# Kernel tuning notes

Hardware: AMD Instinct MI355X
Metric: run time of the kernel (lower is better)

## Reference

```python
import jax, jax.numpy as jnp
import numpy as np
import math

D_MODEL = 768
NUM_HEADS = 8
D_ATT = D_MODEL // NUM_HEADS


def _pos_encoding(S):
    # pe: [S, d_model] sinusoidal, scaled by d_model**-0.5, reshaped to [h, S, d_att]
    position = jnp.arange(S, dtype=jnp.float32)[:, None]                      # [S,1]
    div_term = jnp.exp(jnp.arange(0, D_MODEL, 2, dtype=jnp.float32)
                       * (-math.log(10000.0) / D_MODEL))                      # [d_model/2]
    pe = jnp.zeros((S, D_MODEL), dtype=jnp.float32)
    pe = pe.at[:, 0::2].set(jnp.sin(position * div_term))
    pe = pe.at[:, 1::2].set(jnp.cos(position * div_term))
    pe = pe * (D_MODEL ** -0.5)
    return pe.reshape(S, NUM_HEADS, D_ATT).transpose(1, 0, 2)                 # [h,S,d]


def setup_inputs() -> dict:
    key = jax.random.key(0)
    k1, k2 = jax.random.split(key)
    B, S = 16, 4096
    src = jax.random.normal(k1, (B, S, D_MODEL), dtype=jnp.float32)
    src_key_padding_mask = jnp.zeros((B, S), dtype=bool)  # all valid
    query = jax.random.normal(k2, (NUM_HEADS, D_ATT), dtype=jnp.float32) * (D_ATT ** -0.5)
    return {"src": src, "src_key_padding_mask": src_key_padding_mask, "query": query}


def reference(src, src_key_padding_mask, query):
    B, S, C = src.shape
    key = src.reshape(B, S, NUM_HEADS, D_ATT).transpose(0, 2, 1, 3)          # [B,h,S,d]
    val = key + _pos_encoding(S)[None]                                        # [B,h,S,d]
    scores = jnp.einsum('hd,bhsd->bhs', query, key)                           # [B,h,S]
    scores = jnp.where(src_key_padding_mask[:, None, :], -jnp.inf, scores)
    weights = jax.nn.softmax(scores, axis=-1)                                 # [B,h,S]
    pooled = jnp.einsum('bhsd,bhs->bhd', val, weights)                        # [B,h,d]
    return pooled.reshape(B, NUM_HEADS * D_ATT)                               # [B,C]
```

## Files before the change

kernel.cpp:

```cpp
#include <hip/hip_runtime.h>
#include <math.h>

namespace {
constexpr int kB = 16;
constexpr int kS = 4096;
constexpr int kH = 8;
constexpr int kD = 96;
constexpr int kDM = 768;
constexpr int kNC = 64;
constexpr int kCS = kS / kNC;
constexpr int kRW = kCS / 4;
constexpr int kNSC2 = 32;
constexpr int kS2 = kS / kNSC2;
constexpr float kPeScale = 0.03608439182435161f;
constexpr float kNegLog = -9.210340371976184f / 768.0f;
constexpr float kHalfPi = 1.5707963267948966f;
}

__global__ __launch_bounds__(256)
void attn_pass1(const float* __restrict__ src,
                const unsigned char* __restrict__ mask,
                const float* __restrict__ query,
                float* __restrict__ wsO,
                float* __restrict__ wsL,
                float* __restrict__ wsW)
{
    const int blk = (int)blockIdx.x;
    const int b = blk >> 6;
    const int chunk = blk & (kNC - 1);
    const int t = (int)threadIdx.x;
    const int wave = t >> 6;
    const int lane = t & 63;
    const int h = lane >> 3;

    const float* qf = query + 12 * lane;
    const float4 q0 = *(const float4*)(qf);
    const float4 q1 = *(const float4*)(qf + 4);
    const float4 q2 = *(const float4*)(qf + 8);

    float l = 0.0f;
    float o[12];
#pragma unroll
    for (int k = 0; k < 12; ++k) o[k] = 0.0f;

    const int s0 = chunk * kCS + wave;
    const float* base = src + ((size_t)b * kS + s0) * kDM + 12 * lane;
    const unsigned char* mb = mask + (size_t)b * kS + s0;
    float* wb = wsW + ((size_t)b * kS + s0) * kH + h;

    float4 x0 = *(const float4*)(base);
    float4 x1 = *(const float4*)(base + 4);
    float4 x2 = *(const float4*)(base + 8);
    unsigned char mk = mb[0];

    for (int it = 0; it < kRW; ++it) {
        float4 nx0 = {}, nx1 = {}, nx2 = {};
        unsigned char nmk = 0;
        if (it + 1 < kRW) {
            const float* np = base + (size_t)((it + 1) * 4) * kDM;
            nx0 = *(const float4*)(np);
            nx1 = *(const float4*)(np + 4);
            nx2 = *(const float4*)(np + 8);
            nmk = mb[(it + 1) * 4];
        }

        float pd = x0.x * q0.x + x0.y * q0.y + x0.z * q0.z + x0.w * q0.w
                 + x1.x * q1.x + x1.y * q1.y + x1.z * q1.z + x1.w * q1.w
                 + x2.x * q2.x + x2.y * q2.y + x2.z * q2.z + x2.w * q2.w;
        pd += __shfl_xor(pd, 1, 8);
        pd += __shfl_xor(pd, 2, 8);
        pd += __shfl_xor(pd, 4, 8);

        const float w = mk ? 0.0f : __expf(pd);
        l += w;

        o[0]  = fmaf(w, x0.x, o[0]);
        o[1]  = fmaf(w, x0.y, o[1]);
        o[2]  = fmaf(w, x0.z, o[2]);
        o[3]  = fmaf(w, x0.w, o[3]);
        o[4]  = fmaf(w, x1.x, o[4]);
        o[5]  = fmaf(w, x1.y, o[5]);
        o[6]  = fmaf(w, x1.z, o[6]);
        o[7]  = fmaf(w, x1.w, o[7]);
        o[8]  = fmaf(w, x2.x, o[8]);
        o[9]  = fmaf(w, x2.y, o[9]);
        o[10] = fmaf(w, x2.z, o[10]);
        o[11] = fmaf(w, x2.w, o[11]);

        if ((lane & 7) == 0) wb[(size_t)(it * 4) * kH] = w;

        x0 = nx0; x1 = nx1; x2 = nx2; mk = nmk;
    }

    __shared__ float osum[4][kDM];
    __shared__ float lsum[4][kH];

    float* op = &osum[wave][12 * lane];
    ((float4*)op)[0] = make_float4(o[0], o[1], o[2], o[3]);
    ((float4*)op)[1] = make_float4(o[4], o[5], o[6], o[7]);
    ((float4*)op)[2] = make_float4(o[8], o[9], o[10], o[11]);
    if ((lane & 7) == 0) lsum[wave][h] = l;
    __syncthreads();

    if (t < kDM / 4) {
        const float4 a0 = ((const float4*)&osum[0][0])[t];
        const float4 a1 = ((const float4*)&osum[1][0])[t];
        const float4 a2 = ((const float4*)&osum[2][0])[t];
        const float4 a3 = ((const float4*)&osum[3][0])[t];
        float4 r;
        r.x = a0.x + a1.x + a2.x + a3.x;
        r.y = a0.y + a1.y + a2.y + a3.y;
        r.z = a0.z + a1.z + a2.z + a3.z;
        r.w = a0.w + a1.w + a2.w + a3.w;
        ((float4*)(wsO + (size_t)blk * kDM))[t] = r;
    }
    if (t < kH) {
        wsL[blk * kH + t] = lsum[0][t] + lsum[1][t] + lsum[2][t] + lsum[3][t];
    }
}

__global__ __launch_bounds__(128)
void attn_pe(const float* __restrict__ wsW, float* __restrict__ wsP)
{
    const int blk = (int)blockIdx.x;
    const int sc = blk & (kNSC2 - 1);
    const int bh = blk >> 5;
    const int b = bh >> 3;
    const int h = bh & 7;
    const int c = (int)threadIdx.x;
    if (c >= kD) return;

    const float f = __expf(kNegLog * (float)(h * kD + (c & ~1)));
    const int s0 = sc * kS2;
    float sn, cs;
    __sincosf((float)s0 * f + ((c & 1) ? kHalfPi : 0.0f), &sn, &cs);
    float ds, dc;
    __sincosf(f, &ds, &dc);

    const float* wp = wsW + ((size_t)b * kS + s0) * kH + h;
    float acc = 0.0f;
#pragma unroll 4
    for (int i = 0; i < kS2; ++i) {
        const float w = wp[(size_t)i * kH];
        acc = fmaf(w, sn, acc);
        const float ns = fmaf(sn, dc, cs * ds);
        const float nc = fmaf(cs, dc, -sn * ds);
        sn = ns; cs = nc;
    }
    wsP[(size_t)blk * kD + c] = acc * kPeScale;
}

__global__ __launch_bounds__(128)
void attn_combine(const float* __restrict__ wsO,
                  const float* __restrict__ wsL,
                  const float* __restrict__ wsP,
                  float* __restrict__ out)
{
    const int bh = (int)blockIdx.x;
    const int b = bh >> 3;
    const int h = bh & 7;
    const int t = (int)threadIdx.x;

    float L = 0.0f;
#pragma unroll
    for (int cc = 0; cc < kNC; ++cc) L += wsL[(b * kNC + cc) * kH + h];

    if (t < kD) {
        float acc = 0.0f;
#pragma unroll 8
        for (int cc = 0; cc < kNC; ++cc)
            acc += wsO[(size_t)(b * kNC + cc) * kDM + h * kD + t];
#pragma unroll 8
        for (int sc = 0; sc < kNSC2; ++sc)
            acc += wsP[(size_t)(bh * kNSC2 + sc) * kD + t];
        out[(size_t)bh * kD + t] = acc / L;
    }
}

extern "C" void kernel_launch(void* const* d_in, const int* in_sizes, int n_in,
                              void* d_out, int out_size, void* d_ws, size_t ws_size,
                              hipStream_t stream)
{
    const float* src = (const float*)d_in[0];
    const unsigned char* mask = (const unsigned char*)d_in[1];
    const float* query = (const float*)d_in[2];
    float* out = (float*)d_out;

    float* wsO = (float*)d_ws;
    float* wsL = wsO + (size_t)kB * kNC * kDM;
    float* wsW = wsL + (size_t)kB * kNC * kH;
    float* wsP = wsW + (size_t)kB * kS * kH;

    hipLaunchKernelGGL(attn_pass1,
                       dim3(kB * kNC), dim3(256), 0, stream,
                       src, mask, query, wsO, wsL, wsW);
    hipLaunchKernelGGL(attn_pe,
                       dim3(kB * kH * kNSC2), dim3(128), 0, stream,
                       wsW, wsP);
    hipLaunchKernelGGL(attn_combine,
                       dim3(kB * kH), dim3(128), 0, stream,
                       wsO, wsL, wsP, out);
}
```

Baseline: 298.1 us.

## Fuse positional-encoding accumulation into pass1 and drop the separate PE kernel

```diff
diff --git a/kernel.cpp b/kernel.cpp
--- a/kernel.cpp
+++ b/kernel.cpp
@@ -10,11 +10,8 @@
 constexpr int kNC = 64;
 constexpr int kCS = kS / kNC;
 constexpr int kRW = kCS / 4;
-constexpr int kNSC2 = 32;
-constexpr int kS2 = kS / kNSC2;
 constexpr float kPeScale = 0.03608439182435161f;
 constexpr float kNegLog = -9.210340371976184f / 768.0f;
-constexpr float kHalfPi = 1.5707963267948966f;
 }
 
 __global__ __launch_bounds__(256)
@@ -22,8 +19,7 @@
                 const unsigned char* __restrict__ mask,
                 const float* __restrict__ query,
                 float* __restrict__ wsO,
-                float* __restrict__ wsL,
-                float* __restrict__ wsW)
+                float* __restrict__ wsL)
 {
     const int blk = (int)blockIdx.x;
     const int b = blk >> 6;
@@ -38,15 +34,26 @@
     const float4 q1 = *(const float4*)(qf + 4);
     const float4 q2 = *(const float4*)(qf + 8);
 
+    const int cb = 12 * lane;
+    float f[6], sn[6], cs[6], dsn[6], dcs[6];
+#pragma unroll
+    for (int p = 0; p < 6; ++p)
+        f[p] = __expf(kNegLog * (float)(cb + 2 * p));
+
+    const int s0 = chunk * kCS + wave;
+#pragma unroll
+    for (int p = 0; p < 6; ++p) {
+        __sincosf((float)s0 * f[p], &sn[p], &cs[p]);
+        __sincosf(4.0f * f[p], &dsn[p], &dcs[p]);
+    }
+
     float l = 0.0f;
     float o[12];
 #pragma unroll
     for (int k = 0; k < 12; ++k) o[k] = 0.0f;
 
-    const int s0 = chunk * kCS + wave;
     const float* base = src + ((size_t)b * kS + s0) * kDM + 12 * lane;
     const unsigned char* mb = mask + (size_t)b * kS + s0;
-    float* wb = wsW + ((size_t)b * kS + s0) * kH + h;
 
     float4 x0 = *(const float4*)(base);
     float4 x1 = *(const float4*)(base + 4);
@@ -74,20 +81,25 @@
         const float w = mk ? 0.0f : __expf(pd);
         l += w;
 
-        o[0]  = fmaf(w, x0.x, o[0]);
-        o[1]  = fmaf(w, x0.y, o[1]);
-        o[2]  = fmaf(w, x0.z, o[2]);
-        o[3]  = fmaf(w, x0.w, o[3]);
-        o[4]  = fmaf(w, x1.x, o[4]);
-        o[5]  = fmaf(w, x1.y, o[5]);
-        o[6]  = fmaf(w, x1.z, o[6]);
-        o[7]  = fmaf(w, x1.w, o[7]);
-        o[8]  = fmaf(w, x2.x, o[8]);
-        o[9]  = fmaf(w, x2.y, o[9]);
-        o[10] = fmaf(w, x2.z, o[10]);
-        o[11] = fmaf(w, x2.w, o[11]);
+        o[0]  = fmaf(w, fmaf(sn[0], kPeScale, x0.x), o[0]);
+        o[1]  = fmaf(w, fmaf(cs[0], kPeScale, x0.y), o[1]);
+        o[2]  = fmaf(w, fmaf(sn[1], kPeScale, x0.z), o[2]);
+        o[3]  = fmaf(w, fmaf(cs[1], kPeScale, x0.w), o[3]);
+        o[4]  = fmaf(w, fmaf(sn[2], kPeScale, x1.x), o[4]);
+        o[5]  = fmaf(w, fmaf(cs[2], kPeScale, x1.y), o[5]);
+        o[6]  = fmaf(w, fmaf(sn[3], kPeScale, x1.z), o[6]);
+        o[7]  = fmaf(w, fmaf(cs[3], kPeScale, x1.w), o[7]);
+        o[8]  = fmaf(w, fmaf(sn[4], kPeScale, x2.x), o[8]);
+        o[9]  = fmaf(w, fmaf(cs[4], kPeScale, x2.y), o[9]);
+        o[10] = fmaf(w, fmaf(sn[5], kPeScale, x2.z), o[10]);
+        o[11] = fmaf(w, fmaf(cs[5], kPeScale, x2.w), o[11]);
 
-        if ((lane & 7) == 0) wb[(size_t)(it * 4) * kH] = w;
+#pragma unroll
+        for (int p = 0; p < 6; ++p) {
+            const float ns = fmaf(sn[p], dcs[p], cs[p] * dsn[p]);
+            const float nc = fmaf(cs[p], dcs[p], -sn[p] * dsn[p]);
+            sn[p] = ns; cs[p] = nc;
+        }
 
         x0 = nx0; x1 = nx1; x2 = nx2; mk = nmk;
     }
@@ -119,62 +131,28 @@
     }
 }
 
-__global__ __launch_bounds__(128)
-void attn_pe(const float* __restrict__ wsW, float* __restrict__ wsP)
-{
-    const int blk = (int)blockIdx.x;
-    const int sc = blk & (kNSC2 - 1);
-    const int bh = blk >> 5;
-    const int b = bh >> 3;
-    const int h = bh & 7;
-    const int c = (int)threadIdx.x;
-    if (c >= kD) return;
-
-    const float f = __expf(kNegLog * (float)(h * kD + (c & ~1)));
-    const int s0 = sc * kS2;
-    float sn, cs;
-    __sincosf((float)s0 * f + ((c & 1) ? kHalfPi : 0.0f), &sn, &cs);
-    float ds, dc;
-    __sincosf(f, &ds, &dc);
-
-    const float* wp = wsW + ((size_t)b * kS + s0) * kH + h;
-    float acc = 0.0f;
-#pragma unroll 4
-    for (int i = 0; i < kS2; ++i) {
-        const float w = wp[(size_t)i * kH];
-        acc = fmaf(w, sn, acc);
-        const float ns = fmaf(sn, dc, cs * ds);
-        const float nc = fmaf(cs, dc, -sn * ds);
-        sn = ns; cs = nc;
-    }
-    wsP[(size_t)blk * kD + c] = acc * kPeScale;
-}
-
-__global__ __launch_bounds__(128)
+__global__ __launch_bounds__(768)
 void attn_combine(const float* __restrict__ wsO,
                   const float* __restrict__ wsL,
-                  const float* __restrict__ wsP,
                   float* __restrict__ out)
 {
-    const int bh = (int)blockIdx.x;
-    const int b = bh >> 3;
-    const int h = bh & 7;
-    const int t = (int)threadIdx.x;
+    const int b = (int)blockIdx.x;
+    const int d = (int)threadIdx.x;
 
-    float L = 0.0f;
+    __shared__ float Ls[kH];
+    if (d < kH) {
+        float L = 0.0f;
 #pragma unroll
-    for (int cc = 0; cc < kNC; ++cc) L += wsL[(b * kNC + cc) * kH + h];
+        for (int cc = 0; cc < kNC; ++cc) L += wsL[(b * kNC + cc) * kH + d];
+        Ls[d] = L;
+    }
+    __syncthreads();
 
-    if (t < kD) {
-        float acc = 0.0f;
+    float acc = 0.0f;
 #pragma unroll 8
-        for (int cc = 0; cc < kNC; ++cc)
-            acc += wsO[(size_t)(b * kNC + cc) * kDM + h * kD + t];
-#pragma unroll 8
-        for (int sc = 0; sc < kNSC2; ++sc)
-            acc += wsP[(size_t)(bh * kNSC2 + sc) * kD + t];
-        out[(size_t)bh * kD + t] = acc / L;
-    }
+    for (int cc = 0; cc < kNC; ++cc)
+        acc += wsO[(size_t)(b * kNC + cc) * kDM + d];
+    out[(size_t)b * kDM + d] = acc / Ls[d / kD];
 }
 
 extern "C" void kernel_launch(void* const* d_in, const int* in_sizes, int n_in,
@@ -188,16 +166,11 @@
 
     float* wsO = (float*)d_ws;
     float* wsL = wsO + (size_t)kB * kNC * kDM;
-    float* wsW = wsL + (size_t)kB * kNC * kH;
-    float* wsP = wsW + (size_t)kB * kS * kH;
 
     hipLaunchKernelGGL(attn_pass1,
                        dim3(kB * kNC), dim3(256), 0, stream,
-                       src, mask, query, wsO, wsL, wsW);
-    hipLaunchKernelGGL(attn_pe,
-                       dim3(kB * kH * kNSC2), dim3(128), 0, stream,
-                       wsW, wsP);
+                       src, mask, query, wsO, wsL);
     hipLaunchKernelGGL(attn_combine,
-                       dim3(kB * kH), dim3(128), 0, stream,
-                       wsO, wsL, wsP, out);
+                       dim3(kB), dim3(kDM), 0, stream,
+                       wsO, wsL, out);
 }
```

Result: faster. 280.4 us (-6.0%).
